# Kernel tuning notes

Hardware: AMD Instinct MI355X
Metric: run time of the kernel (lower is better)

The kernel has to match this reference:

```python
import jax, jax.numpy as jnp
import numpy as np

N_PRO, N_WAT, E = 60000, 40000, 1000000
N = N_PRO + N_WAT
IN_DIM, HID, HEADS = 21, 32, 4
EDGE_K, EDGE_DIM = 32, 32
RADIUS_MAX = 5.0
FF_HID, OUT_DIM = 128, 2
HC = HID * HEADS


def setup_inputs() -> dict:
    key = jax.random.key(0)
    ks = jax.random.split(key, 32)

    def glorot(k, shape):
        fan = shape[0] + shape[-1]
        return jax.random.normal(k, shape, jnp.float32) * jnp.sqrt(2.0 / fan)

    inp = {
        'protein_pos': jax.random.normal(ks[0], (N_PRO, 3), jnp.float32),
        'water_pos': jax.random.normal(ks[1], (N_WAT, 3), jnp.float32),
        'protein_features': jax.random.uniform(ks[2], (N_PRO, IN_DIM), jnp.float32),
        'edge_index': jax.random.randint(ks[3], (2, E), 0, N, jnp.int64),
        'gamma': jnp.array([10.0], jnp.float32),
        # feature_emb
        'Wf': glorot(ks[4], (IN_DIM, HID)), 'bf': jnp.zeros((HID,), jnp.float32),
        # edge_emb
        'We': glorot(ks[5], (EDGE_K, EDGE_DIM)), 'be': jnp.zeros((EDGE_DIM,), jnp.float32),
        # conv1 (in: HID)
        'W1': glorot(ks[6], (HID, HC)),
        'att_src1': glorot(ks[7], (HEADS, HID)), 'att_dst1': glorot(ks[8], (HEADS, HID)),
        'Wedge1': glorot(ks[9], (EDGE_DIM, HC)), 'att_edge1': glorot(ks[10], (HEADS, HID)),
        'b1': jnp.zeros((HC,), jnp.float32),
        # conv2 (in: HC)
        'W2': glorot(ks[11], (HC, HC)),
        'att_src2': glorot(ks[12], (HEADS, HID)), 'att_dst2': glorot(ks[13], (HEADS, HID)),
        'Wedge2': glorot(ks[14], (EDGE_DIM, HC)), 'att_edge2': glorot(ks[15], (HEADS, HID)),
        'b2': jnp.zeros((HC,), jnp.float32),
        # mlp
        'Wm1': glorot(ks[16], (HC, FF_HID)), 'bm1': jnp.zeros((FF_HID,), jnp.float32),
        'Wm2': glorot(ks[17], (FF_HID, OUT_DIM)), 'bm2': jnp.zeros((OUT_DIM,), jnp.float32),
    }
    return inp


def gat_conv(h, edge_attr, src, dst, W, att_s, att_d, Wedge, att_e, b):
    # h: [N, Din] -> x: [N, H, C]; edge features only modulate attention logits.
    x = (h @ W).reshape(N, HEADS, HID)
    e = (edge_attr @ Wedge).reshape(-1, HEADS, HID)
    a_s = jnp.einsum('nhc,hc->nh', x, att_s)   # [N,H]
    a_d = jnp.einsum('nhc,hc->nh', x, att_d)   # [N,H]
    a_e = jnp.einsum('ehc,hc->eh', e, att_e)   # [E,H]
    alpha = jax.nn.leaky_relu(a_s[src] + a_d[dst] + a_e, 0.2)  # [E,H]
    # segment softmax over incoming edges of each dst node
    m = jax.ops.segment_max(alpha, dst, num_segments=N)
    m = jnp.where(jnp.isfinite(m), m, 0.0)
    ex = jnp.exp(alpha - m[dst])
    den = jax.ops.segment_sum(ex, dst, num_segments=N)
    coef = ex / (den[dst] + 1e-16)             # [E,H]
    msg = x[src] * coef[:, :, None]            # [E,H,C]
    out = jax.ops.segment_sum(msg, dst, num_segments=N)  # [N,H,C]
    return out.reshape(N, HC) + b


def reference(protein_pos, water_pos, protein_features, edge_index, gamma,
              Wf, bf, We, be,
              W1, att_src1, att_dst1, Wedge1, att_edge1, b1,
              W2, att_src2, att_dst2, Wedge2, att_edge2, b2,
              Wm1, bm1, Wm2, bm2):
    pos = jnp.concatenate([protein_pos, water_pos], axis=0)  # [N,3]
    src, dst = edge_index[0], edge_index[1]
    edge_vec = pos[dst] - pos[src]
    edge_dis = jnp.linalg.norm(edge_vec, axis=-1)            # [E]
    # RBF expansion of distances
    centers = jnp.linspace(0.0, RADIUS_MAX, EDGE_K)
    edge_h = jnp.exp(-gamma[0] * (edge_dis[:, None] - centers[None, :]) ** 2)  # [E,K]
    edge_attr = edge_h @ We + be                             # [E,EDGE_DIM]

    # water nodes get one-hot 'water' feature in last slot
    water_feat = jnp.zeros((N_WAT, IN_DIM), protein_features.dtype).at[:, -1].set(1.0)
    feats = jnp.concatenate([protein_features, water_feat], axis=0)
    h = feats @ Wf + bf                                      # [N,HID]

    h = jax.nn.elu(gat_conv(h, edge_attr, src, dst, W1, att_src1, att_dst1, Wedge1, att_edge1, b1))
    h = jax.nn.elu(gat_conv(h, edge_attr, src, dst, W2, att_src2, att_dst2, Wedge2, att_edge2, b2))

    h = jax.nn.relu(h @ Wm1 + bm1) @ Wm2 + bm2               # [N,OUT_DIM]
    return h[N_PRO:]                                         # water nodes only
```

## Files before the change

### kernel.cpp

```cpp
#include <hip/hip_runtime.h>
#include <hip/hip_fp16.h>
#include <stdint.h>

#define N_PRO 60000
#define N_WAT 40000
#define NN    100000
#define NNP   100032
#define NE    1000000
#define IN_DIM 21
#define HID    32
#define HEADS  4
#define HC     128
#define EDGE_K 32
#define LUTN   2048
#define NH0B  ((NNP * 32) / 256)
#define NBUCK 196
#define EPT   8
#define SCATB ((NE / EPT + 255) / 256)
#define FCAP  6144

typedef _Float16 half8 __attribute__((ext_vector_type(8)));
typedef float    f32x4 __attribute__((ext_vector_type(4)));

__global__ __launch_bounds__(256) void k_small(
    const float* We, const float* be,
    const float* Wedge1, const float* atte1,
    const float* Wedge2, const float* atte2,
    const float* Wf, const float* bfv,
    const float* W1, const float* atts1, const float* attd1,
    float* smallw)
{
    __shared__ float V[2][128];
    int t = threadIdx.x;
    {
        int l = t >> 7, dh = t & 127, d = dh >> 2, h = dh & 3;
        const float* Wg = l ? Wedge2 : Wedge1;
        const float* ae = l ? atte2 : atte1;
        float s = 0.f;
        for (int c = 0; c < HID; c++)
            s += Wg[d * HC + h * HID + c] * ae[h * HID + c];
        V[l][dh] = s;
    }
    __syncthreads();
    {
        int l = t >> 7, kh = t & 127, k = kh >> 2, h = kh & 3;
        float s = 0.f;
        for (int d = 0; d < 32; d++)
            s += We[k * 32 + d] * V[l][d * 4 + h];
        smallw[(l ? 132 : 0) + kh] = s;
    }
    if (t < 8) {
        int l = t >> 2, h = t & 3;
        float s = 0.f;
        for (int d = 0; d < 32; d++)
            s += be[d] * V[l][d * 4 + h];
        smallw[(l ? 260 : 128) + h] = s;
    }
    if (t >= 32 && t < 64) {
        int c = t - 32;
        smallw[264 + c] = Wf[20 * 32 + c] + bfv[c];
    }
    {
        int side = t >> 7;
        int h = (t >> 5) & 3, c = t & 31;
        const float* av = side ? attd1 : atts1;
        float s = 0.f;
        for (int j = 0; j < 32; j++)
            s += W1[c * 128 + h * 32 + j] * av[h * 32 + j];
        smallw[(side ? 424 : 296) + (t & 127)] = s;
    }
}

__global__ __launch_bounds__(256) void k_lut(
    const float* __restrict__ smallw, const float* __restrict__ gamma,
    float* __restrict__ lut)
{
    int e = blockIdx.x * 256 + threadIdx.x;
    if (e >= 2 * LUTN) return;
    int layer = e >> 11, bin = e & (LUTN - 1);
    const float* U = smallw + (layer ? 132 : 0);
    const float* aeb = smallw + (layer ? 260 : 128);
    float dd = bin * (1.0f / 256.0f);
    float g = gamma[0];
    float a0 = aeb[0], a1 = aeb[1], a2 = aeb[2], a3 = aeb[3];
    const float step = 5.0f / 31.0f;
    #pragma unroll
    for (int k = 0; k < EDGE_K; k++) {
        float tt = dd - (float)k * step;
        float r = __expf(-g * tt * tt);
        a0 += r * U[k * 4 + 0];
        a1 += r * U[k * 4 + 1];
        a2 += r * U[k * 4 + 2];
        a3 += r * U[k * 4 + 3];
    }
    *(float4*)&lut[(size_t)e * 4] = make_float4(a0, a1, a2, a3);
}

__global__ __launch_bounds__(256) void k_h0(
    const float* __restrict__ pf, const float* __restrict__ Wf,
    const float* __restrict__ bfv, const float* __restrict__ smallw,
    const int* __restrict__ ei, int* __restrict__ gbh,
    __half* __restrict__ h0, float* __restrict__ asd)
{
    int t = threadIdx.x;
    if (blockIdx.x >= NH0B) {
        __shared__ int lh[256];
        lh[t] = 0;
        __syncthreads();
        int e0 = ((blockIdx.x - NH0B) * 256 + t) * EPT;
        if (e0 < NE) {
            int4 da = *(const int4*)&ei[NE + e0];
            int4 db = *(const int4*)&ei[NE + e0 + 4];
            int ds[8] = {da.x, da.y, da.z, da.w, db.x, db.y, db.z, db.w};
            #pragma unroll
            for (int j = 0; j < EPT; j++)
                if ((unsigned)ds[j] < (unsigned)NN)
                    atomicAdd(&lh[ds[j] >> 9], 1);
        }
        __syncthreads();
        if (t < NBUCK && lh[t]) atomicAdd(&gbh[t], lh[t]);
        return;
    }
    __shared__ float Wfs[IN_DIM * 32];
    __shared__ float bfs[32];
    __shared__ float h0w[32];
    __shared__ float vas[128], vad[128];
    for (int i = t; i < IN_DIM * 32; i += 256) Wfs[i] = Wf[i];
    if (t < 32) { bfs[t] = bfv[t]; h0w[t] = smallw[264 + t]; }
    if (t < 128) vas[t] = smallw[296 + t];
    else         vad[t - 128] = smallw[424 + (t - 128)];
    __syncthreads();
    int id = blockIdx.x * 256 + t;
    int n = id >> 5, c = id & 31;
    if (n >= NNP) return;
    float v;
    if (n < N_PRO) {
        float s = bfs[c];
        for (int k = 0; k < IN_DIM; k++)
            s += pf[n * IN_DIM + k] * Wfs[k * 32 + c];
        v = s;
    } else {
        v = h0w[c];
    }
    h0[(size_t)n * 32 + c] = __float2half(v);
    float ps[4], pd[4];
    #pragma unroll
    for (int h = 0; h < 4; h++) {
        ps[h] = v * vas[h * 32 + c];
        pd[h] = v * vad[h * 32 + c];
    }
    #pragma unroll
    for (int m = 1; m < 32; m <<= 1) {
        #pragma unroll
        for (int h = 0; h < 4; h++) {
            ps[h] += __shfl_xor(ps[h], m, 64);
            pd[h] += __shfl_xor(pd[h], m, 64);
        }
    }
    if ((t & 31) == 0) {
        *(float4*)&asd[(size_t)n * 8]     = make_float4(ps[0], ps[1], ps[2], ps[3]);
        *(float4*)&asd[(size_t)n * 8 + 4] = make_float4(pd[0], pd[1], pd[2], pd[3]);
    }
}

__global__ __launch_bounds__(256) void k_bscan(
    const int* __restrict__ gbh, int* __restrict__ gboff,
    int* __restrict__ gcur, int* __restrict__ offp)
{
    __shared__ int s[256];
    int t = threadIdx.x;
    int v = (t < NBUCK) ? gbh[t] : 0;
    s[t] = v;
    __syncthreads();
    #pragma unroll
    for (int o = 1; o < 256; o <<= 1) {
        int x = (t >= o) ? s[t - o] : 0;
        __syncthreads();
        s[t] += x;
        __syncthreads();
    }
    int ex = s[t] - v;
    if (t < NBUCK) { gboff[t] = ex; gcur[t] = ex; }
    if (t == NBUCK - 1) { gboff[NBUCK] = s[t]; offp[NN] = s[t]; }
}

__global__ __launch_bounds__(256) void k_scat(
    const int* __restrict__ ei, const float* __restrict__ ppos,
    const float* __restrict__ wpos, int* __restrict__ gcur,
    uint2* __restrict__ ebuf2)
{
    __shared__ int lh[256];
    __shared__ int lbase[256];
    int t = threadIdx.x;
    lh[t] = 0;
    __syncthreads();
    int e0 = (blockIdx.x * 256 + t) * EPT;
    int bkt[EPT], rnk[EPT];
    unsigned rec0[EPT], rec1[EPT];
    #pragma unroll
    for (int j = 0; j < EPT; j++) bkt[j] = -1;
    if (e0 < NE) {
        int4 sa = *(const int4*)&ei[e0];
        int4 sb = *(const int4*)&ei[e0 + 4];
        int4 da = *(const int4*)&ei[NE + e0];
        int4 db = *(const int4*)&ei[NE + e0 + 4];
        int ss[8] = {sa.x, sa.y, sa.z, sa.w, sb.x, sb.y, sb.z, sb.w};
        int ds[8] = {da.x, da.y, da.z, da.w, db.x, db.y, db.z, db.w};
        #pragma unroll
        for (int j = 0; j < EPT; j++) {
            int s = ss[j], d = ds[j];
            if ((unsigned)d < (unsigned)NN) {
                const float* ps = (s < N_PRO) ? &ppos[s * 3] : &wpos[(s - N_PRO) * 3];
                const float* pd = (d < N_PRO) ? &ppos[d * 3] : &wpos[(d - N_PRO) * 3];
                float dx = pd[0] - ps[0];
                float dy = pd[1] - ps[1];
                float dz = pd[2] - ps[2];
                float dist = sqrtf(dx * dx + dy * dy + dz * dz);
                unsigned code = (unsigned)fminf(dist * 4096.0f, 32767.0f);
                bkt[j] = d >> 9;
                rec0[j] = ((unsigned)d << 15) | code;
                rec1[j] = (unsigned)s;
                rnk[j] = atomicAdd(&lh[bkt[j]], 1);
            }
        }
    }
    __syncthreads();
    if (t < NBUCK) lbase[t] = lh[t] ? atomicAdd(&gcur[t], lh[t]) : 0;
    __syncthreads();
    #pragma unroll
    for (int j = 0; j < EPT; j++)
        if (bkt[j] >= 0)
            ebuf2[lbase[bkt[j]] + rnk[j]] = make_uint2(rec0[j], rec1[j]);
}

__global__ __launch_bounds__(1024) void k_fine(
    const int* __restrict__ gboff, const uint2* __restrict__ ebuf2,
    const float* __restrict__ lutg, const float* __restrict__ asd,
    int* __restrict__ offp, unsigned* __restrict__ e4,
    float* __restrict__ wb)
{
    __shared__ uint2 eL[FCAP];
    __shared__ int lcnt[512], lexc[512];
    __shared__ int wsum[8];
    int b = blockIdx.x, t = threadIdx.x;
    int beg = gboff[b];
    int nb = gboff[b + 1] - beg;
    bool inl = (nb <= FCAP);
    if (inl)
        for (int i = t; i < nb; i += 1024) eL[i] = ebuf2[beg + i];
    if (t < 512) lcnt[t] = 0;
    __syncthreads();
    for (int i = t; i < nb; i += 1024) {
        uint2 u = inl ? eL[i] : ebuf2[beg + i];
        atomicAdd(&lcnt[(u.x >> 15) & 511], 1);
    }
    __syncthreads();
    if (t < 512) {
        int c = lcnt[t];
        int lane = t & 63;
        int v = c;
        #pragma unroll
        for (int d = 1; d < 64; d <<= 1) {
            int x = __shfl_up(v, d, 64);
            if (lane >= d) v += x;
        }
        if (lane == 63) wsum[t >> 6] = v;
        lexc[t] = v - c;
    }
    __syncthreads();
    if (t < 8) {
        int orig = wsum[t];
        int v = orig;
        #pragma unroll
        for (int d = 1; d < 8; d <<= 1) {
            int x = __shfl_up(v, d, 64);
            if (t >= d) v += x;
        }
        wsum[t] = v - orig;
    }
    __syncthreads();
    if (t < 512) {
        lexc[t] += wsum[t >> 6];
        int node = b * 512 + t;
        if (node < NN) offp[node] = beg + lexc[t];
        lcnt[t] = 0;
    }
    __syncthreads();
    for (int i = t; i < nb; i += 1024) {
        uint2 u = inl ? eL[i] : ebuf2[beg + i];
        int ln = (int)((u.x >> 15) & 511u);
        int r = atomicAdd(&lcnt[ln], 1);
        int p = beg + lexc[ln] + r;
        unsigned code = u.x & 32767u;
        unsigned s = u.y;
        e4[p] = (s << 15) | code;
        int n = (b << 9) + ln;
        float f = fminf((float)code * 0.0625f, (float)(LUTN - 2));
        int i0 = (int)f;
        float fr = f - (float)i0;
        float4 A = *(const float4*)&lutg[(size_t)i0 * 4];
        float4 B = *(const float4*)&lutg[(size_t)(i0 + 1) * 4];
        float4 as4 = *(const float4*)&asd[(size_t)s * 8];
        float4 ad4 = *(const float4*)&asd[(size_t)n * 8 + 4];
        float v0 = as4.x + ad4.x + A.x + (B.x - A.x) * fr;
        float v1 = as4.y + ad4.y + A.y + (B.y - A.y) * fr;
        float v2 = as4.z + ad4.z + A.z + (B.z - A.z) * fr;
        float v3 = as4.w + ad4.w + A.w + (B.w - A.w) * fr;
        v0 = fmaxf(v0, 0.2f * v0);
        v1 = fmaxf(v1, 0.2f * v1);
        v2 = fmaxf(v2, 0.2f * v2);
        v3 = fmaxf(v3, 0.2f * v3);
        *(float4*)&wb[(size_t)p * 4] = make_float4(
            __expf(v0), __expf(v1), __expf(v2), __expf(v3));
    }
}

__global__ __launch_bounds__(256) void k_xm(
    const __half* __restrict__ h, const float* __restrict__ Wg,
    const float* __restrict__ atts, const float* __restrict__ attd,
    __half* __restrict__ x16, float* __restrict__ asd)
{
    __shared__ __half Wt[128 * 136];
    __shared__ float attS[128], attD[128];
    int t = threadIdx.x;
    for (int i = t; i < 128 * 32; i += 256) {
        int c = i & 127, d = (i >> 7) * 4;
        float w0 = Wg[(d + 0) * 128 + c];
        float w1 = Wg[(d + 1) * 128 + c];
        float w2 = Wg[(d + 2) * 128 + c];
        float w3 = Wg[(d + 3) * 128 + c];
        __half2 p0 = __floats2half2_rn(w0, w1);
        __half2 p1 = __floats2half2_rn(w2, w3);
        uint2 pk;
        pk.x = *(unsigned*)&p0;
        pk.y = *(unsigned*)&p1;
        *(uint2*)&Wt[c * 136 + d] = pk;
    }
    if (t < 128) { attS[t] = atts[t]; attD[t] = attd[t]; }
    __syncthreads();
    int wv = t >> 6, lane = t & 63;
    int m16 = lane & 15, quad = lane >> 4;
    int n0 = blockIdx.x * 64 + wv * 16;
    f32x4 acc[8];
    #pragma unroll
    for (int ct = 0; ct < 8; ct++) acc[ct] = (f32x4){0.f, 0.f, 0.f, 0.f};
    #pragma unroll
    for (int ks = 0; ks < 4; ks++) {
        int d0 = ks * 32 + quad * 8;
        half8 bf = *(const half8*)&h[(size_t)(n0 + m16) * 128 + d0];
        #pragma unroll
        for (int ct = 0; ct < 8; ct++) {
            half8 af = *(const half8*)&Wt[(ct * 16 + m16) * 136 + d0];
            acc[ct] = __builtin_amdgcn_mfma_f32_16x16x32_f16(af, bf, acc[ct], 0, 0, 0);
        }
    }
    __half* xrow = &x16[(size_t)(n0 + m16) * 128 + quad * 4];
    float ps[4] = {0.f, 0.f, 0.f, 0.f}, pd[4] = {0.f, 0.f, 0.f, 0.f};
    #pragma unroll
    for (int ct = 0; ct < 8; ct++) {
        f32x4 a = acc[ct];
        __half2 h0p = __floats2half2_rn(a[0], a[1]);
        __half2 h1p = __floats2half2_rn(a[2], a[3]);
        uint2 pk;
        pk.x = *(unsigned*)&h0p;
        pk.y = *(unsigned*)&h1p;
        *(uint2*)&xrow[ct * 16] = pk;
        int cb = ct * 16 + quad * 4;
        int hh = ct >> 1;
        ps[hh] += a[0] * attS[cb] + a[1] * attS[cb + 1]
                + a[2] * attS[cb + 2] + a[3] * attS[cb + 3];
        pd[hh] += a[0] * attD[cb] + a[1] * attD[cb + 1]
                + a[2] * attD[cb + 2] + a[3] * attD[cb + 3];
    }
    #pragma unroll
    for (int hh = 0; hh < 4; hh++) {
        ps[hh] += __shfl_xor(ps[hh], 16, 64);
        ps[hh] += __shfl_xor(ps[hh], 32, 64);
        pd[hh] += __shfl_xor(pd[hh], 16, 64);
        pd[hh] += __shfl_xor(pd[hh], 32, 64);
    }
    if (lane < 16) {
        int n = n0 + m16;
        *(float4*)&asd[(size_t)n * 8]     = make_float4(ps[0], ps[1], ps[2], ps[3]);
        *(float4*)&asd[(size_t)n * 8 + 4] = make_float4(pd[0], pd[1], pd[2], pd[3]);
    }
}

__global__ __launch_bounds__(256) void k_aggz(
    const int* __restrict__ off, const unsigned* __restrict__ e4,
    const float* __restrict__ wb, const __half* __restrict__ h016,
    __half* __restrict__ zbuf)
{
    int t = threadIdx.x;
    int wv = t >> 6, lane = t & 63;
    int g = lane >> 4, q = lane & 15;
    int n = blockIdx.x * 16 + wv * 4 + g;
    int beg = off[n], end = off[n + 1];
    const __half2* x2 = (const __half2*)h016;
    float a0x = 0.f, a0y = 0.f, a1x = 0.f, a1y = 0.f;
    float a2x = 0.f, a2y = 0.f, a3x = 0.f, a3y = 0.f;
    float l0 = 0.f, l1 = 0.f, l2 = 0.f, l3 = 0.f;
    int i = beg;
    for (; i + 3 < end; i += 4) {
        unsigned u0 = e4[i],     u1 = e4[i + 1];
        unsigned u2 = e4[i + 2], u3 = e4[i + 3];
        float4 w0 = *(const float4*)&wb[(size_t)i * 4];
        float4 w1 = *(const float4*)&wb[(size_t)(i + 1) * 4];
        float4 w2 = *(const float4*)&wb[(size_t)(i + 2) * 4];
        float4 w3 = *(const float4*)&wb[(size_t)(i + 3) * 4];
        float2 x0 = __half22float2(x2[(u0 >> 15) * 16u + q]);
        float2 x1 = __half22float2(x2[(u1 >> 15) * 16u + q]);
        float2 x2v = __half22float2(x2[(u2 >> 15) * 16u + q]);
        float2 x3 = __half22float2(x2[(u3 >> 15) * 16u + q]);
        a0x += w0.x * x0.x + w1.x * x1.x + w2.x * x2v.x + w3.x * x3.x;
        a0y += w0.x * x0.y + w1.x * x1.y + w2.x * x2v.y + w3.x * x3.y;
        a1x += w0.y * x0.x + w1.y * x1.x + w2.y * x2v.x + w3.y * x3.x;
        a1y += w0.y * x0.y + w1.y * x1.y + w2.y * x2v.y + w3.y * x3.y;
        a2x += w0.z * x0.x + w1.z * x1.x + w2.z * x2v.x + w3.z * x3.x;
        a2y += w0.z * x0.y + w1.z * x1.y + w2.z * x2v.y + w3.z * x3.y;
        a3x += w0.w * x0.x + w1.w * x1.x + w2.w * x2v.x + w3.w * x3.x;
        a3y += w0.w * x0.y + w1.w * x1.y + w2.w * x2v.y + w3.w * x3.y;
        l0 += (w0.x + w1.x) + (w2.x + w3.x);
        l1 += (w0.y + w1.y) + (w2.y + w3.y);
        l2 += (w0.z + w1.z) + (w2.z + w3.z);
        l3 += (w0.w + w1.w) + (w2.w + w3.w);
    }
    for (; i < end; i++) {
        unsigned u0 = e4[i];
        float4 w0 = *(const float4*)&wb[(size_t)i * 4];
        float2 x0 = __half22float2(x2[(u0 >> 15) * 16u + q]);
        a0x += w0.x * x0.x;  a0y += w0.x * x0.y;
        a1x += w0.y * x0.x;  a1y += w0.y * x0.y;
        a2x += w0.z * x0.x;  a2y += w0.z * x0.y;
        a3x += w0.w * x0.x;  a3y += w0.w * x0.y;
        l0 += w0.x; l1 += w0.y; l2 += w0.z; l3 += w0.w;
    }
    float i0v = 1.0f / (l0 + 1e-16f);
    float i1v = 1.0f / (l1 + 1e-16f);
    float i2v = 1.0f / (l2 + 1e-16f);
    float i3v = 1.0f / (l3 + 1e-16f);
    __half* zr = &zbuf[(size_t)n * 128];
    *(__half2*)&zr[      q * 2] = __floats2half2_rn(a0x * i0v, a0y * i0v);
    *(__half2*)&zr[32  + q * 2] = __floats2half2_rn(a1x * i1v, a1y * i1v);
    *(__half2*)&zr[64  + q * 2] = __floats2half2_rn(a2x * i2v, a2y * i2v);
    *(__half2*)&zr[96  + q * 2] = __floats2half2_rn(a3x * i3v, a3y * i3v);
}

__global__ __launch_bounds__(256) void k_zm(
    const __half* __restrict__ zbuf, const float* __restrict__ W1g,
    const float* __restrict__ b1, __half* __restrict__ hbuf)
{
    __shared__ __half Wt[128 * 40];
    int t = threadIdx.x;
    for (int i = t; i < 128 * 8; i += 256) {
        int c = i & 127, k4 = (i >> 7) * 4;
        float w0 = W1g[(k4 + 0) * 128 + c];
        float w1 = W1g[(k4 + 1) * 128 + c];
        float w2 = W1g[(k4 + 2) * 128 + c];
        float w3 = W1g[(k4 + 3) * 128 + c];
        __half2 p0 = __floats2half2_rn(w0, w1);
        __half2 p1 = __floats2half2_rn(w2, w3);
        uint2 pk;
        pk.x = *(unsigned*)&p0;
        pk.y = *(unsigned*)&p1;
        *(uint2*)&Wt[c * 40 + k4] = pk;
    }
    __syncthreads();
    int wv = t >> 6, lane = t & 63;
    int m16 = lane & 15, quad = lane >> 4;
    int n0 = blockIdx.x * 64 + wv * 16;
    half8 bf[4];
    #pragma unroll
    for (int hh = 0; hh < 4; hh++)
        bf[hh] = *(const half8*)&zbuf[(size_t)(n0 + m16) * 128 + hh * 32 + quad * 8];
    f32x4 acc[8];
    #pragma unroll
    for (int ct = 0; ct < 8; ct++) {
        half8 af = *(const half8*)&Wt[(ct * 16 + m16) * 40 + quad * 8];
        acc[ct] = __builtin_amdgcn_mfma_f32_16x16x32_f16(
            af, bf[ct >> 1], (f32x4){0.f, 0.f, 0.f, 0.f}, 0, 0, 0);
    }
    __half* orow = &hbuf[(size_t)(n0 + m16) * 128 + quad * 4];
    #pragma unroll
    for (int ct = 0; ct < 8; ct++) {
        int cb = ct * 16 + quad * 4;
        float4 bb = *(const float4*)&b1[cb];
        float r0 = acc[ct][0] + bb.x;
        float r1 = acc[ct][1] + bb.y;
        float r2 = acc[ct][2] + bb.z;
        float r3 = acc[ct][3] + bb.w;
        r0 = r0 > 0.f ? r0 : __expf(r0) - 1.0f;
        r1 = r1 > 0.f ? r1 : __expf(r1) - 1.0f;
        r2 = r2 > 0.f ? r2 : __expf(r2) - 1.0f;
        r3 = r3 > 0.f ? r3 : __expf(r3) - 1.0f;
        __half2 ha = __floats2half2_rn(r0, r1);
        __half2 hb = __floats2half2_rn(r2, r3);
        uint2 pk;
        pk.x = *(unsigned*)&ha;
        pk.y = *(unsigned*)&hb;
        *(uint2*)&orow[ct * 16] = pk;
    }
}

__global__ __launch_bounds__(256) void k_agg2(
    const int* __restrict__ off, const unsigned* __restrict__ e4,
    const float* __restrict__ lutg, const float* __restrict__ asd,
    const __half* __restrict__ x16, const float* __restrict__ bias,
    __half* __restrict__ hout)
{
    int t = threadIdx.x;
    int wv = t >> 6, lane = t & 63;
    int g = lane >> 5, q = lane & 31;
    int n = N_PRO + blockIdx.x * 8 + wv * 2 + g;
    int h = q >> 3;
    int beg = off[n], end = off[n + 1];
    float adh = asd[(size_t)n * 8 + 4 + h];
    float ax = 0.f, ay = 0.f, az = 0.f, aw = 0.f, ls = 0.f;
    int i = beg;
    for (; i + 1 < end; i += 2) {
        unsigned u0 = e4[i], u1 = e4[i + 1];
        unsigned s0 = u0 >> 15, s1 = u1 >> 15;
        float f0 = fminf((float)(u0 & 32767u) * 0.0625f, (float)(LUTN - 2));
        float f1 = fminf((float)(u1 & 32767u) * 0.0625f, (float)(LUTN - 2));
        int i00 = (int)f0, i10 = (int)f1;
        float fr0 = f0 - (float)i00, fr1 = f1 - (float)i10;
        float A0 = lutg[i00 * 4 + h], B0 = lutg[(i00 + 1) * 4 + h];
        float A1 = lutg[i10 * 4 + h], B1 = lutg[(i10 + 1) * 4 + h];
        float as0 = asd[(size_t)s0 * 8 + h], as1 = asd[(size_t)s1 * 8 + h];
        float2 r0 = *(const float2*)&x16[(size_t)s0 * 128 + q * 4];
        float2 r1 = *(const float2*)&x16[(size_t)s1 * 128 + q * 4];
        float v0 = as0 + adh + A0 + (B0 - A0) * fr0;
        float v1 = as1 + adh + A1 + (B1 - A1) * fr1;
        v0 = fmaxf(v0, 0.2f * v0);
        v1 = fmaxf(v1, 0.2f * v1);
        float w0 = __expf(v0), w1 = __expf(v1);
        float2 f00 = __half22float2(*(__half2*)&r0.x);
        float2 f01 = __half22float2(*(__half2*)&r0.y);
        float2 f10 = __half22float2(*(__half2*)&r1.x);
        float2 f11 = __half22float2(*(__half2*)&r1.y);
        ax += w0 * f00.x + w1 * f10.x;
        ay += w0 * f00.y + w1 * f10.y;
        az += w0 * f01.x + w1 * f11.x;
        aw += w0 * f01.y + w1 * f11.y;
        ls += w0 + w1;
    }
    if (i < end) {
        unsigned u0 = e4[i];
        unsigned s0 = u0 >> 15;
        float f0 = fminf((float)(u0 & 32767u) * 0.0625f, (float)(LUTN - 2));
        int i00 = (int)f0;
        float fr0 = f0 - (float)i00;
        float A0 = lutg[i00 * 4 + h], B0 = lutg[(i00 + 1) * 4 + h];
        float as0 = asd[(size_t)s0 * 8 + h];
        float2 r0 = *(const float2*)&x16[(size_t)s0 * 128 + q * 4];
        float v0 = as0 + adh + A0 + (B0 - A0) * fr0;
        v0 = fmaxf(v0, 0.2f * v0);
        float w0 = __expf(v0);
        float2 f00 = __half22float2(*(__half2*)&r0.x);
        float2 f01 = __half22float2(*(__half2*)&r0.y);
        ax += w0 * f00.x; ay += w0 * f00.y;
        az += w0 * f01.x; aw += w0 * f01.y;
        ls += w0;
    }
    float inv = 1.0f / (ls + 1e-16f);
    float4 bb = *(const float4*)&bias[q * 4];
    float o0 = ax * inv + bb.x;
    float o1 = ay * inv + bb.y;
    float o2 = az * inv + bb.z;
    float o3 = aw * inv + bb.w;
    o0 = o0 > 0.f ? o0 : __expf(o0) - 1.0f;
    o1 = o1 > 0.f ? o1 : __expf(o1) - 1.0f;
    o2 = o2 > 0.f ? o2 : __expf(o2) - 1.0f;
    o3 = o3 > 0.f ? o3 : __expf(o3) - 1.0f;
    __half2 ha = __floats2half2_rn(o0, o1);
    __half2 hb = __floats2half2_rn(o2, o3);
    uint2 pk;
    pk.x = *(unsigned*)&ha;
    pk.y = *(unsigned*)&hb;
    *(uint2*)&hout[(size_t)n * 128 + q * 4] = pk;
}

__global__ __launch_bounds__(256) void k_mlp(
    const __half* __restrict__ hh, const float* __restrict__ Wm1,
    const float* __restrict__ bm1, const float* __restrict__ Wm2,
    const float* __restrict__ bm2, float* __restrict__ out)
{
    __shared__ __half Wt[128 * 136];
    __shared__ float b1s[128];
    __shared__ float w2s[256];
    int t = threadIdx.x;
    for (int i = t; i < 128 * 32; i += 256) {
        int c = i & 127, d = (i >> 7) * 4;
        float w0 = Wm1[(d + 0) * 128 + c];
        float w1 = Wm1[(d + 1) * 128 + c];
        float w2 = Wm1[(d + 2) * 128 + c];
        float w3 = Wm1[(d + 3) * 128 + c];
        __half2 p0 = __floats2half2_rn(w0, w1);
        __half2 p1 = __floats2half2_rn(w2, w3);
        uint2 pk;
        pk.x = *(unsigned*)&p0;
        pk.y = *(unsigned*)&p1;
        *(uint2*)&Wt[c * 136 + d] = pk;
    }
    if (t < 128) b1s[t] = bm1[t];
    w2s[t] = Wm2[t];
    __syncthreads();
    int wv = t >> 6, lane = t & 63;
    int m16 = lane & 15, quad = lane >> 4;
    int n0 = blockIdx.x * 64 + wv * 16;
    f32x4 acc[8];
    #pragma unroll
    for (int ct = 0; ct < 8; ct++) acc[ct] = (f32x4){0.f, 0.f, 0.f, 0.f};
    #pragma unroll
    for (int ks = 0; ks < 4; ks++) {
        int d0 = ks * 32 + quad * 8;
        half8 bf = *(const half8*)&hh[(size_t)(N_PRO + n0 + m16) * 128 + d0];
        #pragma unroll
        for (int ct = 0; ct < 8; ct++) {
            half8 af = *(const half8*)&Wt[(ct * 16 + m16) * 136 + d0];
            acc[ct] = __builtin_amdgcn_mfma_f32_16x16x32_f16(af, bf, acc[ct], 0, 0, 0);
        }
    }
    float p0 = 0.f, p1 = 0.f;
    #pragma unroll
    for (int ct = 0; ct < 8; ct++) {
        int cb = ct * 16 + quad * 4;
        float4 bb = *(const float4*)&b1s[cb];
        float r0 = fmaxf(acc[ct][0] + bb.x, 0.f);
        float r1 = fmaxf(acc[ct][1] + bb.y, 0.f);
        float r2 = fmaxf(acc[ct][2] + bb.z, 0.f);
        float r3 = fmaxf(acc[ct][3] + bb.w, 0.f);
        p0 += r0 * w2s[(cb + 0) * 2] + r1 * w2s[(cb + 1) * 2]
            + r2 * w2s[(cb + 2) * 2] + r3 * w2s[(cb + 3) * 2];
        p1 += r0 * w2s[(cb + 0) * 2 + 1] + r1 * w2s[(cb + 1) * 2 + 1]
            + r2 * w2s[(cb + 2) * 2 + 1] + r3 * w2s[(cb + 3) * 2 + 1];
    }
    p0 += __shfl_xor(p0, 16, 64);
    p0 += __shfl_xor(p0, 32, 64);
    p1 += __shfl_xor(p1, 16, 64);
    p1 += __shfl_xor(p1, 32, 64);
    if (lane < 16) {
        int wn = n0 + m16;
        *(float2*)&out[(size_t)wn * 2] = make_float2(p0 + bm2[0], p1 + bm2[1]);
    }
}

extern "C" void kernel_launch(void* const* d_in, const int* in_sizes, int n_in,
                              void* d_out, int out_size, void* d_ws, size_t ws_size,
                              hipStream_t stream)
{
    const float* ppos   = (const float*)d_in[0];
    const float* wpos   = (const float*)d_in[1];
    const float* pfeat  = (const float*)d_in[2];
    const int*   ei     = (const int*)d_in[3];
    const float* gamma  = (const float*)d_in[4];
    const float* Wf     = (const float*)d_in[5];
    const float* bfv    = (const float*)d_in[6];
    const float* We     = (const float*)d_in[7];
    const float* be     = (const float*)d_in[8];
    const float* W1     = (const float*)d_in[9];
    const float* atts1  = (const float*)d_in[10];
    const float* attd1  = (const float*)d_in[11];
    const float* Wedge1 = (const float*)d_in[12];
    const float* atte1  = (const float*)d_in[13];
    const float* b1     = (const float*)d_in[14];
    const float* W2     = (const float*)d_in[15];
    const float* atts2  = (const float*)d_in[16];
    const float* attd2  = (const float*)d_in[17];
    const float* Wedge2 = (const float*)d_in[18];
    const float* atte2  = (const float*)d_in[19];
    const float* b2     = (const float*)d_in[20];
    const float* Wm1    = (const float*)d_in[21];
    const float* bm1    = (const float*)d_in[22];
    const float* Wm2    = (const float*)d_in[23];
    const float* bm2    = (const float*)d_in[24];
    float* out = (float*)d_out;

    char* ws = (char*)d_ws;
    size_t o = 0;
    auto alloc = [&](size_t bytes) -> char* {
        char* p = ws + o;
        o += (bytes + 255) & ~(size_t)255;
        return p;
    };
    __half*   h0      = (__half*)alloc((size_t)NNP * 32 * 2);
    __half*   x16     = (__half*)alloc((size_t)NNP * 128 * 2);
    __half*   hbuf    = (__half*)alloc((size_t)NNP * 128 * 2);
    float*    asd     = (float*)alloc((size_t)NNP * 8 * 4);
    float*    wb      = (float*)alloc((size_t)NE * 4 * 4);
    int*      offp    = (int*)alloc((size_t)(NN + 1) * 4);
    unsigned* e4      = (unsigned*)alloc((size_t)NE * 4);
    int*      gbh     = (int*)alloc(256 * 4);
    int*      gboff   = (int*)alloc(256 * 4);
    int*      gcur    = (int*)alloc(256 * 4);
    float*    smallw  = (float*)alloc(4096);
    float*    lutbuf  = (float*)alloc((size_t)2 * LUTN * 4 * 4);
    uint2*    ebuf2   = (uint2*)hbuf;

    hipMemsetAsync(gbh, 0, 256 * 4, stream);
    k_small<<<1, 256, 0, stream>>>(We, be, Wedge1, atte1, Wedge2, atte2, Wf, bfv,
                                   W1, atts1, attd1, smallw);
    k_lut<<<(2 * LUTN + 255) / 256, 256, 0, stream>>>(smallw, gamma, lutbuf);
    k_h0<<<NH0B + SCATB, 256, 0, stream>>>(pfeat, Wf, bfv, smallw, ei, gbh, h0, asd);
    k_bscan<<<1, 256, 0, stream>>>(gbh, gboff, gcur, offp);
    k_scat<<<SCATB, 256, 0, stream>>>(ei, ppos, wpos, gcur, ebuf2);
    k_fine<<<NBUCK, 1024, 0, stream>>>(gboff, ebuf2, lutbuf, asd, offp, e4, wb);
    k_aggz<<<NN / 16, 256, 0, stream>>>(offp, e4, wb, h0, x16);
    k_zm<<<NNP / 64, 256, 0, stream>>>(x16, W1, b1, hbuf);
    k_xm<<<NNP / 64, 256, 0, stream>>>(hbuf, W2, atts2, attd2, x16, asd);
    k_agg2<<<N_WAT / 8, 256, 0, stream>>>(offp, e4, lutbuf + (size_t)LUTN * 4, asd, x16, b2, hbuf);
    k_mlp<<<N_WAT / 64, 256, 0, stream>>>(hbuf, Wm1, bm1, Wm2, bm2, out);
}
```

Before: 310.5 us.

## Drop bucket histogram pass, use fixed-capacity buckets, fuse aggregation with W1 matmul

Removes the destination-bucket histogram and scan kernels. Edges are now scattered into fixed-capacity slots per bucket (FCAP each), and each node gets begin/end offsets instead of a prefix-sum array. The small-weight precompute and the LUT kernel are merged into one launch that also pre-converts W1 to fp16. The first-layer aggregation now applies the W1 MFMA, bias and ELU directly from shared memory, so the z intermediate buffer and the k_zm launch are gone. The aim is fewer launches and less global traffic, but edges silently drop if any bucket exceeds FCAP, and the edge buffers get larger.

```diff
diff --git a/kernel.cpp b/kernel.cpp
--- a/kernel.cpp
+++ b/kernel.cpp
@@ -18,71 +18,108 @@
 #define EPT   8
 #define SCATB ((NE / EPT + 255) / 256)
 #define FCAP  6144
+#define SLOTS (NBUCK * FCAP)
 
 typedef _Float16 half8 __attribute__((ext_vector_type(8)));
 typedef float    f32x4 __attribute__((ext_vector_type(4)));
 
-__global__ __launch_bounds__(256) void k_small(
+__global__ __launch_bounds__(256) void k_pre(
     const float* We, const float* be,
     const float* Wedge1, const float* atte1,
     const float* Wedge2, const float* atte2,
     const float* Wf, const float* bfv,
     const float* W1, const float* atts1, const float* attd1,
-    float* smallw)
+    const float* gamma,
+    float* smallw, float* lut, __half* w1h, int* gcur)
 {
     __shared__ float V[2][128];
+    __shared__ float aebs[4];
     int t = threadIdx.x;
-    {
-        int l = t >> 7, dh = t & 127, d = dh >> 2, h = dh & 3;
-        const float* Wg = l ? Wedge2 : Wedge1;
-        const float* ae = l ? atte2 : atte1;
+    if (blockIdx.x == 16) {
+        {
+            int l = t >> 7, dh = t & 127, d = dh >> 2, h = dh & 3;
+            const float* Wg = l ? Wedge2 : Wedge1;
+            const float* ae = l ? atte2 : atte1;
+            float s = 0.f;
+            for (int c = 0; c < HID; c++)
+                s += Wg[d * HC + h * HID + c] * ae[h * HID + c];
+            V[l][dh] = s;
+        }
+        __syncthreads();
+        {
+            int l = t >> 7, kh = t & 127, k = kh >> 2, h = kh & 3;
+            float s = 0.f;
+            for (int d = 0; d < 32; d++)
+                s += We[k * 32 + d] * V[l][d * 4 + h];
+            smallw[(l ? 132 : 0) + kh] = s;
+        }
+        if (t < 8) {
+            int l = t >> 2, h = t & 3;
+            float s = 0.f;
+            for (int d = 0; d < 32; d++)
+                s += be[d] * V[l][d * 4 + h];
+            smallw[(l ? 260 : 128) + h] = s;
+        }
+        if (t >= 32 && t < 64) {
+            int c = t - 32;
+            smallw[264 + c] = Wf[20 * 32 + c] + bfv[c];
+        }
+        {
+            int side = t >> 7;
+            int h = (t >> 5) & 3, c = t & 31;
+            const float* av = side ? attd1 : atts1;
+            float s = 0.f;
+            for (int j = 0; j < 32; j++)
+                s += W1[c * 128 + h * 32 + j] * av[h * 32 + j];
+            smallw[(side ? 424 : 296) + (t & 127)] = s;
+        }
+        for (int i = t; i < 128 * 8; i += 256) {
+            int c = i & 127, k4 = (i >> 7) * 4;
+            float w0 = W1[(k4 + 0) * 128 + c];
+            float w1v = W1[(k4 + 1) * 128 + c];
+            float w2 = W1[(k4 + 2) * 128 + c];
+            float w3 = W1[(k4 + 3) * 128 + c];
+            __half2 p0 = __floats2half2_rn(w0, w1v);
+            __half2 p1 = __floats2half2_rn(w2, w3);
+            uint2 pk;
+            pk.x = *(unsigned*)&p0;
+            pk.y = *(unsigned*)&p1;
+            *(uint2*)&w1h[c * 40 + k4] = pk;
+        }
+        gcur[t] = 0;
+        return;
+    }
+    int e = blockIdx.x * 256 + t;
+    int layer = e >> 11, bin = e & (LUTN - 1);
+    const float* Wg = layer ? Wedge2 : Wedge1;
+    const float* ae = layer ? atte2 : atte1;
+    if (t < 128) {
+        int d = t >> 2, h = t & 3;
         float s = 0.f;
-        for (int c = 0; c < HID; c++)
+        for (int c = 0; c < 32; c++)
             s += Wg[d * HC + h * HID + c] * ae[h * HID + c];
-        V[l][dh] = s;
-    }
-    __syncthreads();
-    {
-        int l = t >> 7, kh = t & 127, k = kh >> 2, h = kh & 3;
+        V[0][t] = s;
+    }
+    __syncthreads();
+    if (t < 128) {
+        int k = t >> 2, h = t & 3;
         float s = 0.f;
         for (int d = 0; d < 32; d++)
-            s += We[k * 32 + d] * V[l][d * 4 + h];
-        smallw[(l ? 132 : 0) + kh] = s;
-    }
-    if (t < 8) {
-        int l = t >> 2, h = t & 3;
+            s += We[k * 32 + d] * V[0][d * 4 + h];
+        V[1][t] = s;
+    }
+    if (t >= 128 && t < 132) {
+        int h = t - 128;
         float s = 0.f;
         for (int d = 0; d < 32; d++)
-            s += be[d] * V[l][d * 4 + h];
-        smallw[(l ? 260 : 128) + h] = s;
-    }
-    if (t >= 32 && t < 64) {
-        int c = t - 32;
-        smallw[264 + c] = Wf[20 * 32 + c] + bfv[c];
-    }
-    {
-        int side = t >> 7;
-        int h = (t >> 5) & 3, c = t & 31;
-        const float* av = side ? attd1 : atts1;
-        float s = 0.f;
-        for (int j = 0; j < 32; j++)
-            s += W1[c * 128 + h * 32 + j] * av[h * 32 + j];
-        smallw[(side ? 424 : 296) + (t & 127)] = s;
-    }
-}
-
-__global__ __launch_bounds__(256) void k_lut(
-    const float* __restrict__ smallw, const float* __restrict__ gamma,
-    float* __restrict__ lut)
-{
-    int e = blockIdx.x * 256 + threadIdx.x;
-    if (e >= 2 * LUTN) return;
-    int layer = e >> 11, bin = e & (LUTN - 1);
-    const float* U = smallw + (layer ? 132 : 0);
-    const float* aeb = smallw + (layer ? 260 : 128);
+            s += be[d] * V[0][d * 4 + h];
+        aebs[h] = s;
+    }
+    __syncthreads();
+    const float* U = V[1];
     float dd = bin * (1.0f / 256.0f);
     float g = gamma[0];
-    float a0 = aeb[0], a1 = aeb[1], a2 = aeb[2], a3 = aeb[3];
+    float a0 = aebs[0], a1 = aebs[1], a2 = aebs[2], a3 = aebs[3];
     const float step = 5.0f / 31.0f;
     #pragma unroll
     for (int k = 0; k < EDGE_K; k++) {
@@ -99,28 +136,9 @@
 __global__ __launch_bounds__(256) void k_h0(
     const float* __restrict__ pf, const float* __restrict__ Wf,
     const float* __restrict__ bfv, const float* __restrict__ smallw,
-    const int* __restrict__ ei, int* __restrict__ gbh,
     __half* __restrict__ h0, float* __restrict__ asd)
 {
     int t = threadIdx.x;
-    if (blockIdx.x >= NH0B) {
-        __shared__ int lh[256];
-        lh[t] = 0;
-        __syncthreads();
-        int e0 = ((blockIdx.x - NH0B) * 256 + t) * EPT;
-        if (e0 < NE) {
-            int4 da = *(const int4*)&ei[NE + e0];
-            int4 db = *(const int4*)&ei[NE + e0 + 4];
-            int ds[8] = {da.x, da.y, da.z, da.w, db.x, db.y, db.z, db.w};
-            #pragma unroll
-            for (int j = 0; j < EPT; j++)
-                if ((unsigned)ds[j] < (unsigned)NN)
-                    atomicAdd(&lh[ds[j] >> 9], 1);
-        }
-        __syncthreads();
-        if (t < NBUCK && lh[t]) atomicAdd(&gbh[t], lh[t]);
-        return;
-    }
     __shared__ float Wfs[IN_DIM * 32];
     __shared__ float bfs[32];
     __shared__ float h0w[32];
@@ -161,27 +179,6 @@
         *(float4*)&asd[(size_t)n * 8]     = make_float4(ps[0], ps[1], ps[2], ps[3]);
         *(float4*)&asd[(size_t)n * 8 + 4] = make_float4(pd[0], pd[1], pd[2], pd[3]);
     }
-}
-
-__global__ __launch_bounds__(256) void k_bscan(
-    const int* __restrict__ gbh, int* __restrict__ gboff,
-    int* __restrict__ gcur, int* __restrict__ offp)
-{
-    __shared__ int s[256];
-    int t = threadIdx.x;
-    int v = (t < NBUCK) ? gbh[t] : 0;
-    s[t] = v;
-    __syncthreads();
-    #pragma unroll
-    for (int o = 1; o < 256; o <<= 1) {
-        int x = (t >= o) ? s[t - o] : 0;
-        __syncthreads();
-        s[t] += x;
-        __syncthreads();
-    }
-    int ex = s[t] - v;
-    if (t < NBUCK) { gboff[t] = ex; gcur[t] = ex; }
-    if (t == NBUCK - 1) { gboff[NBUCK] = s[t]; offp[NN] = s[t]; }
 }
 
 __global__ __launch_bounds__(256) void k_scat(
@@ -229,34 +226,35 @@
     __syncthreads();
     #pragma unroll
     for (int j = 0; j < EPT; j++)
-        if (bkt[j] >= 0)
-            ebuf2[lbase[bkt[j]] + rnk[j]] = make_uint2(rec0[j], rec1[j]);
+        if (bkt[j] >= 0) {
+            int p = lbase[bkt[j]] + rnk[j];
+            if (p < FCAP)
+                ebuf2[(size_t)bkt[j] * FCAP + p] = make_uint2(rec0[j], rec1[j]);
+        }
 }
 
 __global__ __launch_bounds__(1024) void k_fine(
-    const int* __restrict__ gboff, const uint2* __restrict__ ebuf2,
+    const int* __restrict__ gcur, const uint2* __restrict__ ebuf2,
     const float* __restrict__ lutg, const float* __restrict__ asd,
-    int* __restrict__ offp, unsigned* __restrict__ e4,
-    float* __restrict__ wb)
+    int* __restrict__ offA, int* __restrict__ offE,
+    unsigned* __restrict__ e4, float* __restrict__ wb)
 {
     __shared__ uint2 eL[FCAP];
     __shared__ int lcnt[512], lexc[512];
     __shared__ int wsum[8];
     int b = blockIdx.x, t = threadIdx.x;
-    int beg = gboff[b];
-    int nb = gboff[b + 1] - beg;
-    bool inl = (nb <= FCAP);
-    if (inl)
-        for (int i = t; i < nb; i += 1024) eL[i] = ebuf2[beg + i];
+    int beg = b * FCAP;
+    int nb = gcur[b];
+    if (nb > FCAP) nb = FCAP;
+    for (int i = t; i < nb; i += 1024) eL[i] = ebuf2[beg + i];
     if (t < 512) lcnt[t] = 0;
     __syncthreads();
-    for (int i = t; i < nb; i += 1024) {
-        uint2 u = inl ? eL[i] : ebuf2[beg + i];
-        atomicAdd(&lcnt[(u.x >> 15) & 511], 1);
-    }
-    __syncthreads();
+    for (int i = t; i < nb; i += 1024)
+        atomicAdd(&lcnt[(eL[i].x >> 15) & 511], 1);
+    __syncthreads();
+    int c = 0;
     if (t < 512) {
-        int c = lcnt[t];
+        c = lcnt[t];
         int lane = t & 63;
         int v = c;
         #pragma unroll
@@ -282,12 +280,15 @@
     if (t < 512) {
         lexc[t] += wsum[t >> 6];
         int node = b * 512 + t;
-        if (node < NN) offp[node] = beg + lexc[t];
+        if (node < NN) {
+            offA[node] = beg + lexc[t];
+            offE[node] = beg + lexc[t] + c;
+        }
         lcnt[t] = 0;
     }
     __syncthreads();
     for (int i = t; i < nb; i += 1024) {
-        uint2 u = inl ? eL[i] : ebuf2[beg + i];
+        uint2 u = eL[i];
         int ln = (int)((u.x >> 15) & 511u);
         int r = atomicAdd(&lcnt[ln], 1);
         int p = beg + lexc[ln] + r;
@@ -387,15 +388,23 @@
 }
 
 __global__ __launch_bounds__(256) void k_aggz(
-    const int* __restrict__ off, const unsigned* __restrict__ e4,
-    const float* __restrict__ wb, const __half* __restrict__ h016,
-    __half* __restrict__ zbuf)
-{
+    const int* __restrict__ offA, const int* __restrict__ offE,
+    const unsigned* __restrict__ e4, const float* __restrict__ wb,
+    const __half* __restrict__ h016, const __half* __restrict__ w1h,
+    const float* __restrict__ b1, __half* __restrict__ hbuf)
+{
+    __shared__ __half Wt[128 * 40];
+    __shared__ __half zs[16][136];
     int t = threadIdx.x;
+    {
+        uint4* dst = (uint4*)Wt;
+        const uint4* src = (const uint4*)w1h;
+        for (int i = t; i < 640; i += 256) dst[i] = src[i];
+    }
     int wv = t >> 6, lane = t & 63;
     int g = lane >> 4, q = lane & 15;
     int n = blockIdx.x * 16 + wv * 4 + g;
-    int beg = off[n], end = off[n + 1];
+    int beg = offA[n], end = offE[n];
     const __half2* x2 = (const __half2*)h016;
     float a0x = 0.f, a0y = 0.f, a1x = 0.f, a1y = 0.f;
     float a2x = 0.f, a2y = 0.f, a3x = 0.f, a3y = 0.f;
@@ -439,56 +448,27 @@
     float i1v = 1.0f / (l1 + 1e-16f);
     float i2v = 1.0f / (l2 + 1e-16f);
     float i3v = 1.0f / (l3 + 1e-16f);
-    __half* zr = &zbuf[(size_t)n * 128];
-    *(__half2*)&zr[      q * 2] = __floats2half2_rn(a0x * i0v, a0y * i0v);
-    *(__half2*)&zr[32  + q * 2] = __floats2half2_rn(a1x * i1v, a1y * i1v);
-    *(__half2*)&zr[64  + q * 2] = __floats2half2_rn(a2x * i2v, a2y * i2v);
-    *(__half2*)&zr[96  + q * 2] = __floats2half2_rn(a3x * i3v, a3y * i3v);
-}
-
-__global__ __launch_bounds__(256) void k_zm(
-    const __half* __restrict__ zbuf, const float* __restrict__ W1g,
-    const float* __restrict__ b1, __half* __restrict__ hbuf)
-{
-    __shared__ __half Wt[128 * 40];
-    int t = threadIdx.x;
-    for (int i = t; i < 128 * 8; i += 256) {
-        int c = i & 127, k4 = (i >> 7) * 4;
-        float w0 = W1g[(k4 + 0) * 128 + c];
-        float w1 = W1g[(k4 + 1) * 128 + c];
-        float w2 = W1g[(k4 + 2) * 128 + c];
-        float w3 = W1g[(k4 + 3) * 128 + c];
-        __half2 p0 = __floats2half2_rn(w0, w1);
-        __half2 p1 = __floats2half2_rn(w2, w3);
-        uint2 pk;
-        pk.x = *(unsigned*)&p0;
-        pk.y = *(unsigned*)&p1;
-        *(uint2*)&Wt[c * 40 + k4] = pk;
-    }
-    __syncthreads();
-    int wv = t >> 6, lane = t & 63;
+    int nl = wv * 4 + g;
+    *(__half2*)&zs[nl][     q * 2] = __floats2half2_rn(a0x * i0v, a0y * i0v);
+    *(__half2*)&zs[nl][32 + q * 2] = __floats2half2_rn(a1x * i1v, a1y * i1v);
+    *(__half2*)&zs[nl][64 + q * 2] = __floats2half2_rn(a2x * i2v, a2y * i2v);
+    *(__half2*)&zs[nl][96 + q * 2] = __floats2half2_rn(a3x * i3v, a3y * i3v);
+    __syncthreads();
     int m16 = lane & 15, quad = lane >> 4;
-    int n0 = blockIdx.x * 64 + wv * 16;
-    half8 bf[4];
-    #pragma unroll
-    for (int hh = 0; hh < 4; hh++)
-        bf[hh] = *(const half8*)&zbuf[(size_t)(n0 + m16) * 128 + hh * 32 + quad * 8];
-    f32x4 acc[8];
-    #pragma unroll
-    for (int ct = 0; ct < 8; ct++) {
+    half8 bf = *(const half8*)&zs[m16][wv * 32 + quad * 8];
+    __half* orow = &hbuf[(size_t)(blockIdx.x * 16 + m16) * 128 + quad * 4];
+    #pragma unroll
+    for (int c2 = 0; c2 < 2; c2++) {
+        int ct = wv * 2 + c2;
         half8 af = *(const half8*)&Wt[(ct * 16 + m16) * 40 + quad * 8];
-        acc[ct] = __builtin_amdgcn_mfma_f32_16x16x32_f16(
-            af, bf[ct >> 1], (f32x4){0.f, 0.f, 0.f, 0.f}, 0, 0, 0);
-    }
-    __half* orow = &hbuf[(size_t)(n0 + m16) * 128 + quad * 4];
-    #pragma unroll
-    for (int ct = 0; ct < 8; ct++) {
+        f32x4 acc = __builtin_amdgcn_mfma_f32_16x16x32_f16(
+            af, bf, (f32x4){0.f, 0.f, 0.f, 0.f}, 0, 0, 0);
         int cb = ct * 16 + quad * 4;
         float4 bb = *(const float4*)&b1[cb];
-        float r0 = acc[ct][0] + bb.x;
-        float r1 = acc[ct][1] + bb.y;
-        float r2 = acc[ct][2] + bb.z;
-        float r3 = acc[ct][3] + bb.w;
+        float r0 = acc[0] + bb.x;
+        float r1 = acc[1] + bb.y;
+        float r2 = acc[2] + bb.z;
+        float r3 = acc[3] + bb.w;
         r0 = r0 > 0.f ? r0 : __expf(r0) - 1.0f;
         r1 = r1 > 0.f ? r1 : __expf(r1) - 1.0f;
         r2 = r2 > 0.f ? r2 : __expf(r2) - 1.0f;
@@ -503,7 +483,8 @@
 }
 
 __global__ __launch_bounds__(256) void k_agg2(
-    const int* __restrict__ off, const unsigned* __restrict__ e4,
+    const int* __restrict__ offA, const int* __restrict__ offE,
+    const unsigned* __restrict__ e4,
     const float* __restrict__ lutg, const float* __restrict__ asd,
     const __half* __restrict__ x16, const float* __restrict__ bias,
     __half* __restrict__ hout)
@@ -513,7 +494,7 @@
     int g = lane >> 5, q = lane & 31;
     int n = N_PRO + blockIdx.x * 8 + wv * 2 + g;
     int h = q >> 3;
-    int beg = off[n], end = off[n + 1];
+    int beg = offA[n], end = offE[n];
     float adh = asd[(size_t)n * 8 + 4 + h];
     float ax = 0.f, ay = 0.f, az = 0.f, aw = 0.f, ls = 0.f;
     int i = beg;
@@ -687,27 +668,25 @@
     __half*   x16     = (__half*)alloc((size_t)NNP * 128 * 2);
     __half*   hbuf    = (__half*)alloc((size_t)NNP * 128 * 2);
     float*    asd     = (float*)alloc((size_t)NNP * 8 * 4);
-    float*    wb      = (float*)alloc((size_t)NE * 4 * 4);
-    int*      offp    = (int*)alloc((size_t)(NN + 1) * 4);
-    unsigned* e4      = (unsigned*)alloc((size_t)NE * 4);
-    int*      gbh     = (int*)alloc(256 * 4);
-    int*      gboff   = (int*)alloc(256 * 4);
+    float*    wb      = (float*)alloc((size_t)SLOTS * 4 * 4);
+    int*      offA    = (int*)alloc((size_t)NN * 4);
+    int*      offE    = (int*)alloc((size_t)NN * 4);
+    unsigned* e4      = (unsigned*)alloc((size_t)SLOTS * 4);
     int*      gcur    = (int*)alloc(256 * 4);
     float*    smallw  = (float*)alloc(4096);
     float*    lutbuf  = (float*)alloc((size_t)2 * LUTN * 4 * 4);
+    __half*   w1h     = (__half*)alloc((size_t)128 * 40 * 2);
     uint2*    ebuf2   = (uint2*)hbuf;
 
-    hipMemsetAsync(gbh, 0, 256 * 4, stream);
-    k_small<<<1, 256, 0, stream>>>(We, be, Wedge1, atte1, Wedge2, atte2, Wf, bfv,
-                                   W1, atts1, attd1, smallw);
-    k_lut<<<(2 * LUTN + 255) / 256, 256, 0, stream>>>(smallw, gamma, lutbuf);
-    k_h0<<<NH0B + SCATB, 256, 0, stream>>>(pfeat, Wf, bfv, smallw, ei, gbh, h0, asd);
-    k_bscan<<<1, 256, 0, stream>>>(gbh, gboff, gcur, offp);
+    k_pre<<<17, 256, 0, stream>>>(We, be, Wedge1, atte1, Wedge2, atte2, Wf, bfv,
+                                  W1, atts1, attd1, gamma,
+                                  smallw, lutbuf, w1h, gcur);
+    k_h0<<<NH0B, 256, 0, stream>>>(pfeat, Wf, bfv, smallw, h0, asd);
     k_scat<<<SCATB, 256, 0, stream>>>(ei, ppos, wpos, gcur, ebuf2);
-    k_fine<<<NBUCK, 1024, 0, stream>>>(gboff, ebuf2, lutbuf, asd, offp, e4, wb);
-    k_aggz<<<NN / 16, 256, 0, stream>>>(offp, e4, wb, h0, x16);
-    k_zm<<<NNP / 64, 256, 0, stream>>>(x16, W1, b1, hbuf);
+    k_fine<<<NBUCK, 1024, 0, stream>>>(gcur, ebuf2, lutbuf, asd, offA, offE, e4, wb);
+    k_aggz<<<NN / 16, 256, 0, stream>>>(offA, offE, e4, wb, h0, w1h, b1, hbuf);
     k_xm<<<NNP / 64, 256, 0, stream>>>(hbuf, W2, atts2, attd2, x16, asd);
-    k_agg2<<<N_WAT / 8, 256, 0, stream>>>(offp, e4, lutbuf + (size_t)LUTN * 4, asd, x16, b2, hbuf);
+    k_agg2<<<N_WAT / 8, 256, 0, stream>>>(offA, offE, e4,
+                                          lutbuf + (size_t)LUTN * 4, asd, x16, b2, hbuf);
     k_mlp<<<N_WAT / 64, 256, 0, stream>>>(hbuf, Wm1, bm1, Wm2, bm2, out);
 }
```

Measured after the change: 288.2 us. -7.2%, faster.
